# Optimization experiments

Hardware: AMD Instinct MI355X
Metric: run time of the kernel (lower is better)

Reference implementation:

```python
import jax, jax.numpy as jnp
import numpy as np

C = 256
BN_EPS = 1e-5


def conv1x1(x, w, b):
    # x: (B, Cin, H, W), w: (Cout, Cin), b: (Cout,)
    return jnp.einsum('bchw,oc->bohw', x, w) + b[None, :, None, None]


def setup_inputs() -> dict:
    key = jax.random.key(0)
    ks = jax.random.split(key, 12)
    B, H, W = 8, 64, 64
    s = 1.0 / np.sqrt(C)
    inp = {
        'xi': jax.random.normal(ks[0], (B, C, H, W), jnp.float32),
        'xj': jax.random.normal(ks[1], (B, C, H, W), jnp.float32),
        'g_w': jax.random.normal(ks[2], (C, C), jnp.float32) * s,
        'g_b': jax.random.normal(ks[3], (C,), jnp.float32) * s,
        'theta_w': jax.random.normal(ks[4], (C, C), jnp.float32) * s,
        'theta_b': jax.random.normal(ks[5], (C,), jnp.float32) * s,
        'phi_w': jax.random.normal(ks[6], (C, C), jnp.float32) * s,
        'phi_b': jax.random.normal(ks[7], (C,), jnp.float32) * s,
        'W_w': jax.random.normal(ks[8], (C, C), jnp.float32) * s,
        'W_b': jax.random.normal(ks[9], (C,), jnp.float32) * s,
        'bn_gamma': jnp.ones((C,), jnp.float32),
        'bn_beta': jnp.zeros((C,), jnp.float32),
    }
    return inp


def reference(xi, xj, g_w, g_b, theta_w, theta_b, phi_w, phi_b, W_w, W_b, bn_gamma, bn_beta):
    B, Cc, H, W = xi.shape
    N = H * W
    # 1x1 conv projections, flattened to token sequences
    g_x = conv1x1(xj, g_w, g_b).reshape(B, Cc, N)        # (B, C, N)
    theta_x = conv1x1(xi, theta_w, theta_b).reshape(B, Cc, N)  # (B, C, N)
    phi_x = conv1x1(xj, phi_w, phi_b).reshape(B, Cc, N)  # (B, C, N)
    # f = theta^T @ phi, scaled by N (no softmax)
    f = jnp.einsum('bcn,bcm->bnm', theta_x, phi_x) / N   # (B, N, N)
    # y = f @ g^T, back to channel-first
    y = jnp.einsum('bnm,bcm->bcn', f, g_x).reshape(B, Cc, H, W)
    W_y = conv1x1(y, W_w, W_b)
    z = W_y + xi
    # BatchNorm2d (training-mode batch statistics, biased variance)
    mean = jnp.mean(z, axis=(0, 2, 3), keepdims=True)
    var = jnp.var(z, axis=(0, 2, 3), keepdims=True)
    z_hat = (z - mean) * jax.lax.rsqrt(var + BN_EPS)
    return z_hat * bn_gamma[None, :, None, None] + bn_beta[None, :, None, None]
```

## Files before the change

kernel.cpp:

```cpp
#include <hip/hip_runtime.h>
#include <cstddef>

#define CCH 256
#define NPIX 4096
#define NB 8
#define INVCNT (1.0f/32768.0f)
#define INVN (1.0f/4096.0f)

typedef __bf16 bf16_t;
typedef __attribute__((ext_vector_type(8))) __bf16 bf16x8;
typedef __attribute__((ext_vector_type(4))) __bf16 bf16x4;
typedef __attribute__((ext_vector_type(4))) float f32x4;

#define OFF_S      0u
#define OFF_AB     2048u
#define OFF_BMT    34816u
#define OFF_T1     67584u
#define OFF_R      67840u
#define OFF_W1     68096u
#define OFF_C1     68352u
#define OFF_G      68608u
#define OFF_MP     330752u
#define OFF_E      592896u
#define OFF_RSP    594944u
#define OFF_ZPS    627712u
#define OFF_ZPQ    758784u
#define OFF_SCALE  889856u
#define OFF_SHIFT  890112u
#define OFF_GP     890368u
#define OFF_XIT    5084672u

__device__ __forceinline__ void pack8(const float4& x, const float4& y, bf16x8& o) {
  o[0]=(bf16_t)x.x; o[1]=(bf16_t)x.y; o[2]=(bf16_t)x.z; o[3]=(bf16_t)x.w;
  o[4]=(bf16_t)y.x; o[5]=(bf16_t)y.y; o[6]=(bf16_t)y.z; o[7]=(bf16_t)y.w;
}

__device__ __forceinline__ void ld4(const float* p, float4& a0, float4& a1, float4& a2, float4& a3) {
  a0 = *(const float4*)p;       a1 = *(const float4*)(p + 4);
  a2 = *(const float4*)(p + 8); a3 = *(const float4*)(p + 12);
}

template <bool ATRANS>
__device__ __forceinline__ void mm64v(const float* __restrict__ A,
                                      const float* __restrict__ B,
                                      int i0, int j0,
                                      float (&acc)[2][4],
                                      float (*s1)[65], float (*s2)[65]) {
  const int t = threadIdx.x, tx = t & 15, ty = t >> 4;
  for (int k0 = 0; k0 < 256; k0 += 64) {
#pragma unroll
    for (int it = 0; it < 2; ++it) {
      const int f = t + 512 * it;
      const int row = f >> 4, cc = (f & 15) * 4;
      float4 va;
      if (ATRANS)
        va = *(const float4*)(A + (size_t)(k0 + row) * CCH + i0 + cc);
      else
        va = *(const float4*)(A + (size_t)(i0 + row) * CCH + k0 + cc);
      const float4 vb = *(const float4*)(B + (size_t)(k0 + row) * CCH + j0 + cc);
      s1[row][cc + 0] = va.x; s1[row][cc + 1] = va.y; s1[row][cc + 2] = va.z; s1[row][cc + 3] = va.w;
      s2[row][cc + 0] = vb.x; s2[row][cc + 1] = vb.y; s2[row][cc + 2] = vb.z; s2[row][cc + 3] = vb.w;
    }
    __syncthreads();
#pragma unroll 4
    for (int kk = 0; kk < 64; ++kk) {
      float ar[2], br[4];
#pragma unroll
      for (int i = 0; i < 2; ++i) ar[i] = ATRANS ? s1[kk][2 * ty + i] : s1[2 * ty + i][kk];
#pragma unroll
      for (int j = 0; j < 4; ++j) br[j] = s2[kk][4 * tx + j];
#pragma unroll
      for (int i = 0; i < 2; ++i)
#pragma unroll
        for (int j = 0; j < 4; ++j) acc[i][j] += ar[i] * br[j];
    }
    __syncthreads();
  }
}

__device__ void pre_body(int blk, const float* Ww, const float* gw, const float* phw,
                         const float* thw, const float* gb, const float* phb,
                         const float* thb, float* ws, unsigned char* SMEM) {
  const int t = threadIdx.x;
  if (blk < 32) {
    float (*s1)[65] = (float(*)[65])SMEM;
    float (*s2)[65] = (float(*)[65])(SMEM + 16640);
    const int tb = blk & 15;
    const int i0 = (tb >> 2) * 64, j0 = (tb & 3) * 64;
    float acc[2][4] = {};
    if (blk < 16) mm64v<false>(Ww, gw, i0, j0, acc, s1, s2);
    else          mm64v<true >(thw, phw, i0, j0, acc, s1, s2);
    bf16_t* outp = (bf16_t*)(ws + (blk < 16 ? OFF_AB : OFF_BMT));
    const int tx = t & 15, ty = t >> 4;
#pragma unroll
    for (int i = 0; i < 2; ++i) {
      bf16x4 mv;
#pragma unroll
      for (int q = 0; q < 4; ++q) mv[q] = (bf16_t)acc[i][q];
      *(bf16x4*)&outp[(size_t)(i0 + 2 * ty + i) * CCH + j0 + 4 * tx] = mv;
    }
  } else {
    if (t < 256) {
      float t1v = 0.f, rv = 0.f, w1v = 0.f;
      for (int k = 0; k < 256; ++k) {
        t1v += phw[k * CCH + t] * thb[k];
        rv  += thw[k * CCH + t] * phb[k];
        w1v += Ww[t * CCH + k] * gb[k];
      }
      ws[OFF_T1 + t] = t1v; ws[OFF_R + t] = rv; ws[OFF_W1 + t] = w1v;
    }
    float* red = (float*)SMEM;
    red[t] = (t < 256) ? phb[t] * thb[t] : 0.f;
    __syncthreads();
    for (int off = 256; off; off >>= 1) { if (t < off) red[t] += red[t + off]; __syncthreads(); }
    if (t == 0) ws[OFF_C1] = red[0];
  }
}

__device__ void cvtT_body(int bx, int b, const float* __restrict__ xi,
                          float* __restrict__ ws, unsigned char* SMEM) {
  bf16_t (*st)[72] = (bf16_t(*)[72])SMEM;
  const int c0 = (bx & 1) * 128;
  const int n0 = (bx >> 1) * 64;
  const float* X = xi + (size_t)b * CCH * NPIX;
  const int t = threadIdx.x;
  const int r = t >> 2, c4 = (t & 3) * 16;
  {
    float4 a0, a1, a2, a3;
    ld4(X + (size_t)(c0 + r) * NPIX + n0 + c4, a0, a1, a2, a3);
    bf16x8 u0, u1;
    pack8(a0, a1, u0); pack8(a2, a3, u1);
    *(bf16x8*)&st[r][c4] = u0;
    *(bf16x8*)&st[r][c4 + 8] = u1;
  }
  __syncthreads();
  bf16_t* Xit = (bf16_t*)(ws + OFF_XIT) + (size_t)b * NPIX * CCH;
  const int nr = t >> 3, cc = (t & 7) * 16;
  bf16x8 o0, o1;
#pragma unroll
  for (int j = 0; j < 8; ++j) o0[j] = st[cc + j][nr];
#pragma unroll
  for (int j = 0; j < 8; ++j) o1[j] = st[cc + 8 + j][nr];
  *(bf16x8*)(Xit + (size_t)(n0 + nr) * CCH + c0 + cc) = o0;
  *(bf16x8*)(Xit + (size_t)(n0 + nr) * CCH + c0 + cc + 8) = o1;
}

__device__ void gram_body(int ks, int b, const float* __restrict__ xj,
                          float* __restrict__ ws, unsigned char* SMEM) {
  const float* __restrict__ X = xj + (size_t)b * CCH * NPIX;
  bf16_t (*sA)[256][40] = (bf16_t(*)[256][40])SMEM;
  const int t = threadIdx.x;
  const int w = t >> 6, lane = t & 63;
  const int wr = w >> 1, wc = w & 1;
  const int lr = lane & 15, hi = lane >> 4;
  const int fcol = 8 * hi;
  const f32x4 z4 = {0.f, 0.f, 0.f, 0.f};
  f32x4 acc[4][8];
#pragma unroll
  for (int fr = 0; fr < 4; ++fr)
#pragma unroll
    for (int fc = 0; fc < 8; ++fc) acc[fr][fc] = z4;
  float rsum = 0.f;
  const int k0 = ks * 256;
  const int srow = t >> 1, sh16 = (t & 1) * 16;

  float4 a0, a1, a2, a3;
  auto LOAD = [&](int kc) {
    ld4(X + (size_t)srow * NPIX + k0 + kc + sh16, a0, a1, a2, a3);
    rsum += a0.x + a0.y + a0.z + a0.w + a1.x + a1.y + a1.z + a1.w
          + a2.x + a2.y + a2.z + a2.w + a3.x + a3.y + a3.z + a3.w;
  };
  auto WRITE = [&](int q) {
    bf16x8 u0, u1;
    pack8(a0, a1, u0); pack8(a2, a3, u1);
    *(bf16x8*)&sA[q][srow][sh16] = u0;
    *(bf16x8*)&sA[q][srow][sh16 + 8] = u1;
  };

  LOAD(0);
  WRITE(0);
  __syncthreads();
  int cur = 0;
  for (int kc8 = 0; kc8 < 8; ++kc8) {
    if (kc8 < 7) LOAD(32 * (kc8 + 1));
    bf16x8 af[4];
#pragma unroll
    for (int fr = 0; fr < 4; ++fr)
      af[fr] = *(const bf16x8*)&sA[cur][64 * wr + 16 * fr + lr][fcol];
#pragma unroll
    for (int fc = 0; fc < 8; ++fc) {
      const bf16x8 bv = *(const bf16x8*)&sA[cur][128 * wc + 16 * fc + lr][fcol];
#pragma unroll
      for (int fr = 0; fr < 4; ++fr)
        acc[fr][fc] = __builtin_amdgcn_mfma_f32_16x16x32_bf16(af[fr], bv, acc[fr][fc], 0, 0, 0);
    }
    if (kc8 < 7) WRITE(cur ^ 1);
    __syncthreads();
    cur ^= 1;
  }

  {
    const float o = __shfl_down(rsum, 1);
    if (!(t & 1)) ws[OFF_RSP + ((size_t)(b * 16 + ks)) * CCH + srow] = rsum + o;
  }
  bf16_t* GPp = (bf16_t*)(ws + OFF_GP) + (size_t)(b * 16 + ks) * 65536;
#pragma unroll
  for (int fr = 0; fr < 4; ++fr)
#pragma unroll
    for (int fc = 0; fc < 8; ++fc)
#pragma unroll
      for (int reg = 0; reg < 4; ++reg)
        GPp[(size_t)(64 * wr + 16 * fr + 4 * hi + reg) * CCH + 128 * wc + 16 * fc + lr] =
            (bf16_t)acc[fr][fc][reg];
}

__global__ __launch_bounds__(512) void k_mega(const float* __restrict__ xi,
                                              const float* __restrict__ xj,
                                              const float* __restrict__ Ww,
                                              const float* __restrict__ gw,
                                              const float* __restrict__ phw,
                                              const float* __restrict__ thw,
                                              const float* __restrict__ gb,
                                              const float* __restrict__ phb,
                                              const float* __restrict__ thb,
                                              float* __restrict__ ws) {
  __shared__ __align__(16) unsigned char SMEM[40960];
  const int bx = blockIdx.x, by = blockIdx.y;
  if (bx >= 144) {
    if (by == 0) pre_body(bx - 144, Ww, gw, phw, thw, gb, phb, thb, ws, SMEM);
    return;
  }
  if (bx >= 16) { cvtT_body(bx - 16, by, xi, ws, SMEM); return; }
  gram_body(bx, by, xj, ws, SMEM);
}

__global__ __launch_bounds__(256) void k_greduce(float* __restrict__ ws) {
  const int b = blockIdx.y, bx = blockIdx.x, t = threadIdx.x;
  const bf16_t* GPp = (const bf16_t*)(ws + OFF_GP) + (size_t)b * 16 * 65536;
  bf16_t* Gb = (bf16_t*)(ws + OFF_G) + (size_t)b * 65536;
  const int row = bx * 8 + (t >> 5);
  const int j8 = (t & 31) * 8;
  float s[8] = {};
#pragma unroll
  for (int ks = 0; ks < 16; ++ks) {
    const bf16x8 v = *(const bf16x8*)&GPp[(size_t)ks * 65536 + row * CCH + j8];
#pragma unroll
    for (int q = 0; q < 8; ++q) s[q] += (float)v[q];
  }
  bf16x8 o;
#pragma unroll
  for (int q = 0; q < 8; ++q) o[q] = (bf16_t)s[q];
  *(bf16x8*)&Gb[(size_t)row * CCH + j8] = o;
  if (t < 128) {
    const int rr = bx * 8 + (t >> 4), l = t & 15;
    float v = ws[OFF_RSP + ((size_t)(b * 16 + l)) * CCH + rr];
#pragma unroll
    for (int off = 8; off; off >>= 1) v += __shfl_down(v, off, 16);
    if (l == 0) ws[OFF_S + b * CCH + rr] = v;
  }
}

__global__ __launch_bounds__(256) void k_kmmat(const float* __restrict__ Wb, float* __restrict__ ws) {
  const int b = blockIdx.y;
  const int i0 = blockIdx.x * 32;
  const int t = threadIdx.x;
  const int w = t >> 6, lane = t & 63;
  const int rg = w >> 1, cg = w & 1;
  const int lr = lane & 15, hi = lane >> 4;
  const int fcol = 8 * hi;

  __shared__ __align__(16) bf16_t sA[2][32][40];
  __shared__ __align__(16) bf16_t sB[2][256][40];
  __shared__ __align__(16) bf16_t sK[32][264];
  __shared__ float sS[256], sT1[256], sR[256], sW1[256], sVS[256];
  __shared__ float sU[32];
  __shared__ float red[256];
  __shared__ float sdt_sh;

  const bf16_t* Ab  = (const bf16_t*)(ws + OFF_AB);
  const bf16_t* BmT = (const bf16_t*)(ws + OFF_BMT);
  const bf16_t* Gb  = (const bf16_t*)(ws + OFF_G) + (size_t)b * 65536;

  sS[t]  = ws[OFF_S + b * CCH + t];
  sT1[t] = ws[OFF_T1 + t];
  sR[t]  = ws[OFF_R + t];
  sW1[t] = ws[OFF_W1 + t];
  __syncthreads();
  red[t] = sS[t] * sT1[t];
  __syncthreads();
  for (int off = 128; off; off >>= 1) { if (t < off) red[t] += red[t + off]; __syncthreads(); }
  if (t == 0) sdt_sh = red[0];
  {
    float a = 0.f;
    for (int k8 = 0; k8 < 256; k8 += 8) {
      const bf16x8 v = *(const bf16x8*)&BmT[(size_t)t * CCH + k8];
#pragma unroll
      for (int q = 0; q < 8; ++q) a += (float)v[q] * sS[k8 + q];
    }
    sVS[t] = a;
  }
  if (t < 32) {
    float a = 0.f;
    for (int k8 = 0; k8 < 256; k8 += 8) {
      const bf16x8 v = *(const bf16x8*)&Ab[(size_t)(i0 + t) * CCH + k8];
#pragma unroll
      for (int q = 0; q < 8; ++q) a += (float)v[q] * sS[k8 + q];
    }
    sU[t] = a;
  }

  const f32x4 z4 = {0.f, 0.f, 0.f, 0.f};
  const int arow = t >> 2, achk = (t & 3) * 8;
  const int arA = t >> 2, akA = (t & 3) * 8;

  f32x4 acc[8];
#pragma unroll
  for (int fc = 0; fc < 8; ++fc) acc[fc] = z4;
  bf16x8 ra;
  bf16x8 gb8[4];
  auto LOADB = [&](int k) {
    if (t < 128) ra = *(const bf16x8*)&Ab[(size_t)(i0 + arA) * CCH + k + akA];
#pragma unroll
    for (int h = 0; h < 4; ++h)
      gb8[h] = *(const bf16x8*)&Gb[(size_t)(64 * h + arow) * CCH + k + achk];
  };
  auto WRITEB = [&](int q) {
    if (t < 128) *(bf16x8*)&sA[q][arA][akA] = ra;
#pragma unroll
    for (int h = 0; h < 4; ++h)
      *(bf16x8*)&sB[q][64 * h + arow][achk] = gb8[h];
  };
  LOADB(0);
  WRITEB(0);
  __syncthreads();
  int cur = 0;
  for (int ks = 0; ks < 8; ++ks) {
    if (ks < 7) LOADB(32 * (ks + 1));
    const bf16x8 af = *(const bf16x8*)&sA[cur][16 * rg + lr][fcol];
#pragma unroll
    for (int fc = 0; fc < 8; ++fc) {
      const bf16x8 bv = *(const bf16x8*)&sB[cur][128 * cg + 16 * fc + lr][fcol];
      acc[fc] = __builtin_amdgcn_mfma_f32_16x16x32_bf16(af, bv, acc[fc], 0, 0, 0);
    }
    if (ks < 7) WRITEB(cur ^ 1);
    __syncthreads();
    cur ^= 1;
  }
#pragma unroll
  for (int fc = 0; fc < 8; ++fc)
#pragma unroll
    for (int reg = 0; reg < 4; ++reg)
      sK[16 * rg + 4 * hi + reg][128 * cg + 16 * fc + lr] = (bf16_t)acc[fc][reg];
  __syncthreads();

  if (t < 32) {
    float dot = 0.f;
    for (int k8 = 0; k8 < 256; k8 += 8) {
      const bf16x8 v = *(const bf16x8*)&sK[t][k8];
#pragma unroll
      for (int q = 0; q < 8; ++q) dot += (float)v[q] * sT1[k8 + q];
    }
    const float c1 = ws[OFF_C1];
    const float ui = sU[t], w1i = sW1[i0 + t];
    ws[OFF_E + b * CCH + i0 + t] = INVN * (dot + c1 * ui + sdt_sh * w1i) + c1 * w1i + Wb[i0 + t];
  }

  f32x4 acc2[8];
#pragma unroll
  for (int fc = 0; fc < 8; ++fc) acc2[fc] = z4;
  bf16x8 rb[4];
  auto LOADC = [&](int k) {
#pragma unroll
    for (int h = 0; h < 4; ++h)
      rb[h] = *(const bf16x8*)&BmT[(size_t)(64 * h + arow) * CCH + k + achk];
  };
  auto WRITEC = [&](int q) {
#pragma unroll
    for (int h = 0; h < 4; ++h)
      *(bf16x8*)&sB[q][64 * h + arow][achk] = rb[h];
  };
  LOADC(0);
  WRITEC(0);
  __syncthreads();
  cur = 0;
  for (int ks = 0; ks < 8; ++ks) {
    if (ks < 7) LOADC(32 * (ks + 1));
    const bf16x8 af = *(const bf16x8*)&sK[16 * rg + lr][32 * ks + fcol];
#pragma unroll
    for (int fc = 0; fc < 8; ++fc) {
      const bf16x8 bv = *(const bf16x8*)&sB[cur][128 * cg + 16 * fc + lr][fcol];
      acc2[fc] = __builtin_amdgcn_mfma_f32_16x16x32_bf16(af, bv, acc2[fc], 0, 0, 0);
    }
    if (ks < 7) WRITEC(cur ^ 1);
    __syncthreads();
    cur ^= 1;
  }

  bf16_t* Mp = (bf16_t*)(ws + OFF_MP) + (size_t)b * 65536;
#pragma unroll
  for (int fc = 0; fc < 8; ++fc) {
    const int j = 128 * cg + 16 * fc + lr;
    const float rj = sR[j], vsj = sVS[j];
#pragma unroll
    for (int reg = 0; reg < 4; ++reg) {
      const int il = 16 * rg + 4 * hi + reg;
      const float ui = sU[il], w1i = sW1[i0 + il];
      float m = (acc2[fc][reg] + ui * rj + w1i * vsj) * INVN + w1i * rj;
      if (i0 + il == j) m += 1.0f;
      Mp[(size_t)(i0 + il) * CCH + j] = (bf16_t)m;
    }
  }
}

template <int APPLY>
__global__ __launch_bounds__(256) void k_zmm(float* __restrict__ ws, float* __restrict__ out) {
  const int b = blockIdx.y, nblk = blockIdx.x;
  const int n0 = nblk * 64;
  const int t = threadIdx.x;
  const int w = t >> 6, lane = t & 63;
  const int rg = w >> 1, cg = w & 1;
  __shared__ __align__(16) bf16_t sA[2][64][40];
  __shared__ __align__(16) bf16_t sB[2][256][40];
  __shared__ float sC1[256], sC2[256];
  __shared__ float redS[4][128], redQ[4][128];
  {
    const float e = ws[OFF_E + b * CCH + t];
    if (APPLY) {
      const float sc = ws[OFF_SCALE + t];
      sC1[t] = sc;
      sC2[t] = e * sc + ws[OFF_SHIFT + t];
    } else {
      sC1[t] = e;
    }
  }
  const bf16_t* Xit = (const bf16_t*)(ws + OFF_XIT) + (size_t)b * NPIX * CCH;
  const bf16_t* Mp = (const bf16_t*)(ws + OFF_MP) + (size_t)b * 65536;
  const f32x4 z4 = {0.f, 0.f, 0.f, 0.f};
  f32x4 acc[2][8];
#pragma unroll
  for (int fr = 0; fr < 2; ++fr)
#pragma unroll
    for (int fc = 0; fc < 8; ++fc) acc[fr][fc] = z4;
  const int arow = t >> 2, achk = (t & 3) * 8;
  bf16x8 ra, rb0, rb1, rb2, rb3;
  ra  = *(const bf16x8*)(Xit + (size_t)(n0 + arow) * CCH + achk);
  rb0 = *(const bf16x8*)(Mp + (size_t)(arow)       * CCH + achk);
  rb1 = *(const bf16x8*)(Mp + (size_t)(64 + arow)  * CCH + achk);
  rb2 = *(const bf16x8*)(Mp + (size_t)(128 + arow) * CCH + achk);
  rb3 = *(const bf16x8*)(Mp + (size_t)(192 + arow) * CCH + achk);
  *(bf16x8*)&sA[0][arow][achk] = ra;
  *(bf16x8*)&sB[0][arow][achk] = rb0;
  *(bf16x8*)&sB[0][64 + arow][achk] = rb1;
  *(bf16x8*)&sB[0][128 + arow][achk] = rb2;
  *(bf16x8*)&sB[0][192 + arow][achk] = rb3;
  __syncthreads();
  int cur = 0;
  for (int ks = 0; ks < 8; ++ks) {
    const int nk = 32 * (ks + 1);
    if (ks < 7) {
      ra  = *(const bf16x8*)(Xit + (size_t)(n0 + arow) * CCH + nk + achk);
      rb0 = *(const bf16x8*)(Mp + (size_t)(arow)       * CCH + nk + achk);
      rb1 = *(const bf16x8*)(Mp + (size_t)(64 + arow)  * CCH + nk + achk);
      rb2 = *(const bf16x8*)(Mp + (size_t)(128 + arow) * CCH + nk + achk);
      rb3 = *(const bf16x8*)(Mp + (size_t)(192 + arow) * CCH + nk + achk);
    }
    const int fcol = 8 * (lane >> 4);
    const int lr = lane & 15;
    const bf16x8 af0 = *(const bf16x8*)&sA[cur][32 * rg + lr][fcol];
    const bf16x8 af1 = *(const bf16x8*)&sA[cur][32 * rg + 16 + lr][fcol];
#pragma unroll
    for (int fc = 0; fc < 8; ++fc) {
      const bf16x8 bv = *(const bf16x8*)&sB[cur][128 * cg + 16 * fc + lr][fcol];
      acc[0][fc] = __builtin_amdgcn_mfma_f32_16x16x32_bf16(af0, bv, acc[0][fc], 0, 0, 0);
      acc[1][fc] = __builtin_amdgcn_mfma_f32_16x16x32_bf16(af1, bv, acc[1][fc], 0, 0, 0);
    }
    if (ks < 7) {
      *(bf16x8*)&sA[cur ^ 1][arow][achk] = ra;
      *(bf16x8*)&sB[cur ^ 1][arow][achk] = rb0;
      *(bf16x8*)&sB[cur ^ 1][64 + arow][achk] = rb1;
      *(bf16x8*)&sB[cur ^ 1][128 + arow][achk] = rb2;
      *(bf16x8*)&sB[cur ^ 1][192 + arow][achk] = rb3;
    }
    __syncthreads();
    cur ^= 1;
  }
  if (APPLY) {
#pragma unroll
    for (int fc = 0; fc < 8; ++fc) {
      const int c = 128 * cg + 16 * fc + (lane & 15);
      const float sc = sC1[c], b2 = sC2[c];
      float* op = out + ((size_t)b * CCH + c) * NPIX + n0 + 32 * rg + ((lane >> 4) << 2);
#pragma unroll
      for (int fr = 0; fr < 2; ++fr) {
        float4 v;
        v.x = acc[fr][fc][0] * sc + b2;
        v.y = acc[fr][fc][1] * sc + b2;
        v.z = acc[fr][fc][2] * sc + b2;
        v.w = acc[fr][fc][3] * sc + b2;
        *(float4*)(op + 16 * fr) = v;
      }
    }
  } else {
    float ps[8], pq[8];
#pragma unroll
    for (int fc = 0; fc < 8; ++fc) {
      const int c = 128 * cg + 16 * fc + (lane & 15);
      const float e = sC1[c];
      float s = 0.f, q = 0.f;
#pragma unroll
      for (int fr = 0; fr < 2; ++fr)
#pragma unroll
        for (int reg = 0; reg < 4; ++reg) {
          const float z = acc[fr][fc][reg] + e;
          s += z; q += z * z;
        }
      s += __shfl_xor(s, 16); s += __shfl_xor(s, 32);
      q += __shfl_xor(q, 16); q += __shfl_xor(q, 32);
      ps[fc] = s; pq[fc] = q;
    }
    if (lane < 16) {
#pragma unroll
      for (int fc = 0; fc < 8; ++fc) {
        redS[w][16 * fc + lane] = ps[fc];
        redQ[w][16 * fc + lane] = pq[fc];
      }
    }
    __syncthreads();
    if (t < 256) {
      const int cg2 = t >> 7, c = t & 127;
      float s = 0.f, q = 0.f;
#pragma unroll
      for (int rg2 = 0; rg2 < 2; ++rg2) {
        s += redS[rg2 * 2 + cg2][c];
        q += redQ[rg2 * 2 + cg2][c];
      }
      ws[OFF_ZPS + (size_t)t * 512 + b * 64 + nblk] = s;
      ws[OFF_ZPQ + (size_t)t * 512 + b * 64 + nblk] = q;
    }
  }
}

__global__ __launch_bounds__(64) void k_bnstats(const float* __restrict__ gamma,
                                                const float* __restrict__ beta,
                                                float* __restrict__ ws) {
  const int c = blockIdx.x, t = threadIdx.x;
  const float* PS = ws + OFF_ZPS + (size_t)c * 512;
  const float* PQ = ws + OFF_ZPQ + (size_t)c * 512;
  float s = 0.f, q = 0.f;
#pragma unroll
  for (int e = 0; e < 8; ++e) { s += PS[t + 64 * e]; q += PQ[t + 64 * e]; }
#pragma unroll
  for (int off = 32; off; off >>= 1) { s += __shfl_down(s, off); q += __shfl_down(q, off); }
  if (t == 0) {
    const float mean = s * INVCNT;
    const float var = q * INVCNT - mean * mean;
    const float sc = gamma[c] * rsqrtf(var + 1e-5f);
    ws[OFF_SCALE + c] = sc;
    ws[OFF_SHIFT + c] = beta[c] - mean * sc;
  }
}

extern "C" void kernel_launch(void* const* d_in, const int* in_sizes, int n_in,
                              void* d_out, int out_size, void* d_ws, size_t ws_size,
                              hipStream_t stream) {
  const float* xi  = (const float*)d_in[0];
  const float* xj  = (const float*)d_in[1];
  const float* gw  = (const float*)d_in[2];
  const float* gb  = (const float*)d_in[3];
  const float* thw = (const float*)d_in[4];
  const float* thb = (const float*)d_in[5];
  const float* phw = (const float*)d_in[6];
  const float* phb = (const float*)d_in[7];
  const float* Ww  = (const float*)d_in[8];
  const float* Wb  = (const float*)d_in[9];
  const float* gamma = (const float*)d_in[10];
  const float* beta  = (const float*)d_in[11];
  float* ws = (float*)d_ws;
  float* out = (float*)d_out;

  k_mega<<<dim3(177, 8), 512, 0, stream>>>(xi, xj, Ww, gw, phw, thw, gb, phb, thb, ws);
  k_greduce<<<dim3(32, 8), 256, 0, stream>>>(ws);
  k_kmmat<<<dim3(8, 8), 256, 0, stream>>>(Wb, ws);
  k_zmm<0><<<dim3(64, 8), 256, 0, stream>>>(ws, out);
  k_bnstats<<<256, 64, 0, stream>>>(gamma, beta, ws);
  k_zmm<1><<<dim3(64, 8), 256, 0, stream>>>(ws, out);
}
```

Baseline: 87.46 us.

## Compute BatchNorm statistics analytically from xi Gram matrix instead of extra GEMM pass

The full z = M·xi GEMM pass used only to accumulate per-channel sums and squares is dropped. BN moments are now derived algebraically: the Gram matrix and row sums of xi are computed alongside those of xj in the mega kernel, and k_kmmat computes diag(M·Gx·Mᵀ) for the second moment. A new small kernel turns these into scale/shift. This removes one full 512-block GEMM over xi and its partial-sum traffic, but adds xi Gram work (16 more blocks per batch), a bigger reduction, and a bf16-precision variance computed from sums that may lose accuracy.

Result: slower. 100.5 us (+14.9%).

```diff
diff --git a/kernel.cpp b/kernel.cpp
--- a/kernel.cpp
+++ b/kernel.cpp
@@ -13,22 +13,25 @@
 typedef __attribute__((ext_vector_type(4))) float f32x4;
 
 #define OFF_S      0u
-#define OFF_AB     2048u
-#define OFF_BMT    34816u
-#define OFF_T1     67584u
-#define OFF_R      67840u
-#define OFF_W1     68096u
-#define OFF_C1     68352u
-#define OFF_G      68608u
-#define OFF_MP     330752u
-#define OFF_E      592896u
-#define OFF_RSP    594944u
-#define OFF_ZPS    627712u
-#define OFF_ZPQ    758784u
-#define OFF_SCALE  889856u
-#define OFF_SHIFT  890112u
-#define OFF_GP     890368u
-#define OFF_XIT    5084672u
+#define OFF_SI     2048u
+#define OFF_AB     4096u
+#define OFF_BMT    36864u
+#define OFF_T1     69632u
+#define OFF_R      69888u
+#define OFF_W1     70144u
+#define OFF_C1     70400u
+#define OFF_G      70656u
+#define OFF_GX     332800u
+#define OFF_MP     594944u
+#define OFF_E      857088u
+#define OFF_D      859136u
+#define OFF_RSP    861184u
+#define OFF_RSPX   893952u
+#define OFF_SCALE  926720u
+#define OFF_SHIFT  926976u
+#define OFF_GP     927232u
+#define OFF_GPX    5121536u
+#define OFF_XIT    9315840u
 
 __device__ __forceinline__ void pack8(const float4& x, const float4& y, bf16x8& o) {
   o[0]=(bf16_t)x.x; o[1]=(bf16_t)x.y; o[2]=(bf16_t)x.z; o[3]=(bf16_t)x.w;
@@ -145,9 +148,9 @@
   *(bf16x8*)(Xit + (size_t)(n0 + nr) * CCH + c0 + cc + 8) = o1;
 }
 
-__device__ void gram_body(int ks, int b, const float* __restrict__ xj,
-                          float* __restrict__ ws, unsigned char* SMEM) {
-  const float* __restrict__ X = xj + (size_t)b * CCH * NPIX;
+__device__ void gram_body(int ks, int b, const float* __restrict__ X,
+                          float* __restrict__ ws, unsigned char* SMEM,
+                          unsigned gp_off, unsigned rsp_off) {
   bf16_t (*sA)[256][40] = (bf16_t(*)[256][40])SMEM;
   const int t = threadIdx.x;
   const int w = t >> 6, lane = t & 63;
@@ -201,9 +204,9 @@
 
   {
     const float o = __shfl_down(rsum, 1);
-    if (!(t & 1)) ws[OFF_RSP + ((size_t)(b * 16 + ks)) * CCH + srow] = rsum + o;
-  }
-  bf16_t* GPp = (bf16_t*)(ws + OFF_GP) + (size_t)(b * 16 + ks) * 65536;
+    if (!(t & 1)) ws[rsp_off + ((size_t)(b * 16 + ks)) * CCH + srow] = rsum + o;
+  }
+  bf16_t* GPp = (bf16_t*)(ws + gp_off) + (size_t)(b * 16 + ks) * 65536;
 #pragma unroll
   for (int fr = 0; fr < 4; ++fr)
 #pragma unroll
@@ -226,19 +229,24 @@
                                               float* __restrict__ ws) {
   __shared__ __align__(16) unsigned char SMEM[40960];
   const int bx = blockIdx.x, by = blockIdx.y;
-  if (bx >= 144) {
-    if (by == 0) pre_body(bx - 144, Ww, gw, phw, thw, gb, phb, thb, ws, SMEM);
+  if (bx >= 160) {
+    if (by == 0) pre_body(bx - 160, Ww, gw, phw, thw, gb, phb, thb, ws, SMEM);
     return;
   }
-  if (bx >= 16) { cvtT_body(bx - 16, by, xi, ws, SMEM); return; }
-  gram_body(bx, by, xj, ws, SMEM);
+  if (bx >= 32) { cvtT_body(bx - 32, by, xi, ws, SMEM); return; }
+  if (bx < 16)
+    gram_body(bx, by, xj + (size_t)by * CCH * NPIX, ws, SMEM, OFF_GP, OFF_RSP);
+  else
+    gram_body(bx - 16, by, xi + (size_t)by * CCH * NPIX, ws, SMEM, OFF_GPX, OFF_RSPX);
 }
 
 __global__ __launch_bounds__(256) void k_greduce(float* __restrict__ ws) {
   const int b = blockIdx.y, bx = blockIdx.x, t = threadIdx.x;
-  const bf16_t* GPp = (const bf16_t*)(ws + OFF_GP) + (size_t)b * 16 * 65536;
-  bf16_t* Gb = (bf16_t*)(ws + OFF_G) + (size_t)b * 65536;
-  const int row = bx * 8 + (t >> 5);
+  const bool isX = bx >= 32;
+  const int bxl = bx & 31;
+  const bf16_t* GPp = (const bf16_t*)(ws + (isX ? OFF_GPX : OFF_GP)) + (size_t)b * 16 * 65536;
+  bf16_t* Gb = (bf16_t*)(ws + (isX ? OFF_GX : OFF_G)) + (size_t)b * 65536;
+  const int row = bxl * 8 + (t >> 5);
   const int j8 = (t & 31) * 8;
   float s[8] = {};
 #pragma unroll
@@ -252,11 +260,11 @@
   for (int q = 0; q < 8; ++q) o[q] = (bf16_t)s[q];
   *(bf16x8*)&Gb[(size_t)row * CCH + j8] = o;
   if (t < 128) {
-    const int rr = bx * 8 + (t >> 4), l = t & 15;
-    float v = ws[OFF_RSP + ((size_t)(b * 16 + l)) * CCH + rr];
+    const int rr = bxl * 8 + (t >> 4), l = t & 15;
+    float v = ws[(isX ? OFF_RSPX : OFF_RSP) + ((size_t)(b * 16 + l)) * CCH + rr];
 #pragma unroll
     for (int off = 8; off; off >>= 1) v += __shfl_down(v, off, 16);
-    if (l == 0) ws[OFF_S + b * CCH + rr] = v;
+    if (l == 0) ws[(isX ? OFF_SI : OFF_S) + b * CCH + rr] = v;
   }
 }
 
@@ -275,11 +283,13 @@
   __shared__ float sS[256], sT1[256], sR[256], sW1[256], sVS[256];
   __shared__ float sU[32];
   __shared__ float red[256];
+  __shared__ float redD[2][32];
   __shared__ float sdt_sh;
 
   const bf16_t* Ab  = (const bf16_t*)(ws + OFF_AB);
   const bf16_t* BmT = (const bf16_t*)(ws + OFF_BMT);
   const bf16_t* Gb  = (const bf16_t*)(ws + OFF_G) + (size_t)b * 65536;
+  const bf16_t* Gxb = (const bf16_t*)(ws + OFF_GX) + (size_t)b * 65536;
 
   sS[t]  = ws[OFF_S + b * CCH + t];
   sT1[t] = ws[OFF_T1 + t];
@@ -311,7 +321,6 @@
 
   const f32x4 z4 = {0.f, 0.f, 0.f, 0.f};
   const int arow = t >> 2, achk = (t & 3) * 8;
-  const int arA = t >> 2, akA = (t & 3) * 8;
 
   f32x4 acc[8];
 #pragma unroll
@@ -319,13 +328,13 @@
   bf16x8 ra;
   bf16x8 gb8[4];
   auto LOADB = [&](int k) {
-    if (t < 128) ra = *(const bf16x8*)&Ab[(size_t)(i0 + arA) * CCH + k + akA];
+    if (t < 128) ra = *(const bf16x8*)&Ab[(size_t)(i0 + arow) * CCH + k + achk];
 #pragma unroll
     for (int h = 0; h < 4; ++h)
       gb8[h] = *(const bf16x8*)&Gb[(size_t)(64 * h + arow) * CCH + k + achk];
   };
   auto WRITEB = [&](int q) {
-    if (t < 128) *(bf16x8*)&sA[q][arA][akA] = ra;
+    if (t < 128) *(bf16x8*)&sA[q][arow][achk] = ra;
 #pragma unroll
     for (int h = 0; h < 4; ++h)
       *(bf16x8*)&sB[q][64 * h + arow][achk] = gb8[h];
@@ -397,6 +406,7 @@
   }
 
   bf16_t* Mp = (bf16_t*)(ws + OFF_MP) + (size_t)b * 65536;
+  float mreg[8][4];
 #pragma unroll
   for (int fc = 0; fc < 8; ++fc) {
     const int j = 128 * cg + 16 * fc + lr;
@@ -407,13 +417,99 @@
       const float ui = sU[il], w1i = sW1[i0 + il];
       float m = (acc2[fc][reg] + ui * rj + w1i * vsj) * INVN + w1i * rj;
       if (i0 + il == j) m += 1.0f;
-      Mp[(size_t)(i0 + il) * CCH + j] = (bf16_t)m;
-    }
-  }
-}
-
-template <int APPLY>
-__global__ __launch_bounds__(256) void k_zmm(float* __restrict__ ws, float* __restrict__ out) {
+      const bf16_t mb = (bf16_t)m;
+      Mp[(size_t)(i0 + il) * CCH + j] = mb;
+      mreg[fc][reg] = (float)mb;
+    }
+  }
+#pragma unroll
+  for (int fc = 0; fc < 8; ++fc)
+#pragma unroll
+    for (int reg = 0; reg < 4; ++reg)
+      sK[16 * rg + 4 * hi + reg][128 * cg + 16 * fc + lr] = (bf16_t)mreg[fc][reg];
+  __syncthreads();
+
+  f32x4 acc3[8];
+#pragma unroll
+  for (int fc = 0; fc < 8; ++fc) acc3[fc] = z4;
+  auto LOADD = [&](int k) {
+#pragma unroll
+    for (int h = 0; h < 4; ++h)
+      gb8[h] = *(const bf16x8*)&Gxb[(size_t)(64 * h + arow) * CCH + k + achk];
+  };
+  auto WRITED = [&](int q) {
+#pragma unroll
+    for (int h = 0; h < 4; ++h)
+      *(bf16x8*)&sB[q][64 * h + arow][achk] = gb8[h];
+  };
+  LOADD(0);
+  WRITED(0);
+  __syncthreads();
+  cur = 0;
+  for (int ks = 0; ks < 8; ++ks) {
+    if (ks < 7) LOADD(32 * (ks + 1));
+    const bf16x8 af = *(const bf16x8*)&sK[16 * rg + lr][32 * ks + fcol];
+#pragma unroll
+    for (int fc = 0; fc < 8; ++fc) {
+      const bf16x8 bv = *(const bf16x8*)&sB[cur][128 * cg + 16 * fc + lr][fcol];
+      acc3[fc] = __builtin_amdgcn_mfma_f32_16x16x32_bf16(af, bv, acc3[fc], 0, 0, 0);
+    }
+    if (ks < 7) WRITED(cur ^ 1);
+    __syncthreads();
+    cur ^= 1;
+  }
+  float dpart[4] = {};
+#pragma unroll
+  for (int fc = 0; fc < 8; ++fc)
+#pragma unroll
+    for (int reg = 0; reg < 4; ++reg)
+      dpart[reg] += acc3[fc][reg] * mreg[fc][reg];
+#pragma unroll
+  for (int reg = 0; reg < 4; ++reg) {
+    float d = dpart[reg];
+    d += __shfl_xor(d, 1); d += __shfl_xor(d, 2);
+    d += __shfl_xor(d, 4); d += __shfl_xor(d, 8);
+    dpart[reg] = d;
+  }
+  if (lr == 0) {
+#pragma unroll
+    for (int reg = 0; reg < 4; ++reg)
+      redD[cg][16 * rg + 4 * hi + reg] = dpart[reg];
+  }
+  __syncthreads();
+  if (t < 32) ws[OFF_D + b * CCH + i0 + t] = redD[0][t] + redD[1][t];
+}
+
+__global__ __launch_bounds__(64) void k_bnfin(const float* __restrict__ gamma,
+                                              const float* __restrict__ beta,
+                                              float* __restrict__ ws) {
+  const int c = blockIdx.x, t = threadIdx.x;
+  __shared__ float sSI[NB][256];
+  for (int i = t; i < NB * 256; i += 64) sSI[i >> 8][i & 255] = ws[OFF_SI + i];
+  __syncthreads();
+  float sz = 0.f, sq = 0.f;
+  for (int b = 0; b < NB; ++b) {
+    const bf16_t* Mrow = (const bf16_t*)(ws + OFF_MP) + (size_t)b * 65536 + (size_t)c * CCH;
+    const bf16x4 v = *(const bf16x4*)&Mrow[t * 4];
+    float p = 0.f;
+#pragma unroll
+    for (int q = 0; q < 4; ++q) p += (float)v[q] * sSI[b][t * 4 + q];
+#pragma unroll
+    for (int off = 1; off < 64; off <<= 1) p += __shfl_xor(p, off);
+    const float e = ws[OFF_E + b * CCH + c];
+    sz += p + 4096.f * e;
+    sq += ws[OFF_D + b * CCH + c] + 2.f * e * p + 4096.f * e * e;
+  }
+  if (t == 0) {
+    const float mean = sz * INVCNT;
+    const float var = sq * INVCNT - mean * mean;
+    const float sc = gamma[c] * rsqrtf(var + 1e-5f);
+    ws[OFF_SCALE + c] = sc;
+    ws[OFF_SHIFT + c] = beta[c] - mean * sc;
+  }
+}
+
+__global__ __launch_bounds__(256) void k_zapply(float* __restrict__ ws, float* __restrict__ out) {
   const int b = blockIdx.y, nblk = blockIdx.x;
   const int n0 = nblk * 64;
   const int t = threadIdx.x;
@@ -422,16 +518,11 @@
   __shared__ __align__(16) bf16_t sA[2][64][40];
   __shared__ __align__(16) bf16_t sB[2][256][40];
   __shared__ float sC1[256], sC2[256];
-  __shared__ float redS[4][128], redQ[4][128];
   {
     const float e = ws[OFF_E + b * CCH + t];
-    if (APPLY) {
-      const float sc = ws[OFF_SCALE + t];
-      sC1[t] = sc;
-      sC2[t] = e * sc + ws[OFF_SHIFT + t];
-    } else {
-      sC1[t] = e;
-    }
+    const float sc = ws[OFF_SCALE + t];
+    sC1[t] = sc;
+    sC2[t] = e * sc + ws[OFF_SHIFT + t];
   }
   const bf16_t* Xit = (const bf16_t*)(ws + OFF_XIT) + (size_t)b * NPIX * CCH;
   const bf16_t* Mp = (const bf16_t*)(ws + OFF_MP) + (size_t)b * 65536;
@@ -484,79 +575,20 @@
     __syncthreads();
     cur ^= 1;
   }
-  if (APPLY) {
-#pragma unroll
-    for (int fc = 0; fc < 8; ++fc) {
-      const int c = 128 * cg + 16 * fc + (lane & 15);
-      const float sc = sC1[c], b2 = sC2[c];
-      float* op = out + ((size_t)b * CCH + c) * NPIX + n0 + 32 * rg + ((lane >> 4) << 2);
-#pragma unroll
-      for (int fr = 0; fr < 2; ++fr) {
-        float4 v;
-        v.x = acc[fr][fc][0] * sc + b2;
-        v.y = acc[fr][fc][1] * sc + b2;
-        v.z = acc[fr][fc][2] * sc + b2;
-        v.w = acc[fr][fc][3] * sc + b2;
-        *(float4*)(op + 16 * fr) = v;
-      }
-    }
-  } else {
-    float ps[8], pq[8];
-#pragma unroll
-    for (int fc = 0; fc < 8; ++fc) {
-      const int c = 128 * cg + 16 * fc + (lane & 15);
-      const float e = sC1[c];
-      float s = 0.f, q = 0.f;
-#pragma unroll
-      for (int fr = 0; fr < 2; ++fr)
-#pragma unroll
-        for (int reg = 0; reg < 4; ++reg) {
-          const float z = acc[fr][fc][reg] + e;
-          s += z; q += z * z;
-        }
-      s += __shfl_xor(s, 16); s += __shfl_xor(s, 32);
-      q += __shfl_xor(q, 16); q += __shfl_xor(q, 32);
-      ps[fc] = s; pq[fc] = q;
-    }
-    if (lane < 16) {
-#pragma unroll
-      for (int fc = 0; fc < 8; ++fc) {
-        redS[w][16 * fc + lane] = ps[fc];
-        redQ[w][16 * fc + lane] = pq[fc];
-      }
-    }
-    __syncthreads();
-    if (t < 256) {
-      const int cg2 = t >> 7, c = t & 127;
-      float s = 0.f, q = 0.f;
-#pragma unroll
-      for (int rg2 = 0; rg2 < 2; ++rg2) {
-        s += redS[rg2 * 2 + cg2][c];
-        q += redQ[rg2 * 2 + cg2][c];
-      }
-      ws[OFF_ZPS + (size_t)t * 512 + b * 64 + nblk] = s;
-      ws[OFF_ZPQ + (size_t)t * 512 + b * 64 + nblk] = q;
-    }
-  }
-}
-
-__global__ __launch_bounds__(64) void k_bnstats(const float* __restrict__ gamma,
-                                                const float* __restrict__ beta,
-                                                float* __restrict__ ws) {
-  const int c = blockIdx.x, t = threadIdx.x;
-  const float* PS = ws + OFF_ZPS + (size_t)c * 512;
-  const float* PQ = ws + OFF_ZPQ + (size_t)c * 512;
-  float s = 0.f, q = 0.f;
-#pragma unroll
-  for (int e = 0; e < 8; ++e) { s += PS[t + 64 * e]; q += PQ[t + 64 * e]; }
-#pragma unroll
-  for (int off = 32; off; off >>= 1) { s += __shfl_down(s, off); q += __shfl_down(q, off); }
-  if (t == 0) {
-    const float mean = s * INVCNT;
-    const float var = q * INVCNT - mean * mean;
-    const float sc = gamma[c] * rsqrtf(var + 1e-5f);
-    ws[OFF_SCALE + c] = sc;
-    ws[OFF_SHIFT + c] = beta[c] - mean * sc;
+#pragma unroll
+  for (int fc = 0; fc < 8; ++fc) {
+    const int c = 128 * cg + 16 * fc + (lane & 15);
+    const float sc = sC1[c], b2 = sC2[c];
+    float* op = out + ((size_t)b * CCH + c) * NPIX + n0 + 32 * rg + ((lane >> 4) << 2);
+#pragma unroll
+    for (int fr = 0; fr < 2; ++fr) {
+      float4 v;
+      v.x = acc[fr][fc][0] * sc + b2;
+      v.y = acc[fr][fc][1] * sc + b2;
+      v.z = acc[fr][fc][2] * sc + b2;
+      v.w = acc[fr][fc][3] * sc + b2;
+      *(float4*)(op + 16 * fr) = v;
+    }
   }
 }
 
@@ -578,10 +610,9 @@
   float* ws = (float*)d_ws;
   float* out = (float*)d_out;
 
-  k_mega<<<dim3(177, 8), 512, 0, stream>>>(xi, xj, Ww, gw, phw, thw, gb, phb, thb, ws);
-  k_greduce<<<dim3(32, 8), 256, 0, stream>>>(ws);
+  k_mega<<<dim3(193, 8), 512, 0, stream>>>(xi, xj, Ww, gw, phw, thw, gb, phb, thb, ws);
+  k_greduce<<<dim3(64, 8), 256, 0, stream>>>(ws);
   k_kmmat<<<dim3(8, 8), 256, 0, stream>>>(Wb, ws);
-  k_zmm<0><<<dim3(64, 8), 256, 0, stream>>>(ws, out);
-  k_bnstats<<<256, 64, 0, stream>>>(gamma, beta, ws);
-  k_zmm<1><<<dim3(64, 8), 256, 0, stream>>>(ws, out);
-}
+  k_bnfin<<<256, 64, 0, stream>>>(gamma, beta, ws);
+  k_zapply<<<dim3(64, 8), 256, 0, stream>>>(ws, out);
+}
```
